# Kernel tuning notes

Measured on AMD Instinct MI355X. Metric: run time of the kernel, lower is better.

Reference implementation:

```python
import jax, jax.numpy as jnp
import numpy as np

N_HEAD = 16


def setup_inputs() -> dict:
    key = jax.random.key(0)
    ks = jax.random.split(key, 5)
    B, T, C = 4, 2048, 1024
    s = 0.02
    x = jax.random.normal(ks[0], (B, T, C), jnp.float32)
    wq = jax.random.normal(ks[1], (C, C), jnp.float32) * s
    wk = jax.random.normal(ks[2], (C, C), jnp.float32) * s
    wv = jax.random.normal(ks[3], (C, C), jnp.float32) * s
    wp = jax.random.normal(ks[4], (C, C), jnp.float32) * s
    zb = jnp.zeros((C,), jnp.float32)
    return {"x": x, "wq": wq, "bq": zb, "wk": wk, "bk": zb,
            "wv": wv, "bv": zb, "wp": wp, "bp": zb}


def _rope_cos_sin(T, D):
    half = D // 2
    i = jnp.arange(half, dtype=jnp.float32)
    alpha = 1.0 / (10000.0 ** (2.0 * i / D))        # [half]
    ang = jnp.arange(T, dtype=jnp.float32)[:, None] * alpha  # [T, half]
    return jnp.cos(ang), jnp.sin(ang)


def _apply_rope(t, cos, sin):
    # t: [B, H, T, D]; non-interleaved halves as in the torch module
    half = t.shape[-1] // 2
    xr, xi = t[..., :half], t[..., half:]
    return jnp.concatenate([xr * cos - xi * sin, xr * sin + xi * cos], axis=-1)


def reference(x, wq, bq, wk, bk, wv, bv, wp, bp):
    B, T, C = x.shape
    H = N_HEAD
    D = C // H
    # QKV projections (torch Linear: x @ W.T + b)
    def heads(w, b):
        return (x @ w.T + b).reshape(B, T, H, D).transpose(0, 2, 1, 3)
    q, k, v = heads(wq, bq), heads(wk, bk), heads(wv, bv)
    cos, sin = _rope_cos_sin(T, D)  # each [T, D//2], broadcasts over B,H
    q = _apply_rope(q, cos, sin)
    k = _apply_rope(k, cos, sin)
    scale = 1.0 / np.sqrt(D).astype(np.float32)
    att = jnp.einsum('bhtd,bhsd->bhts', q, k) * scale  # [B,H,T,T]
    causal = jnp.tril(jnp.ones((T, T), bool))
    att = jnp.where(causal, att, jnp.float32(-jnp.inf))
    att = jax.nn.softmax(att, axis=-1)
    y = jnp.einsum('bhts,bhsd->bhtd', att, v)  # [B,H,T,D]
    y = y.transpose(0, 2, 1, 3).reshape(B, T, C)
    return y @ wp.T + bp
```

## Files before the change

### kernel.cpp

```cpp
#include <hip/hip_runtime.h>
#include <math.h>

constexpr int B = 4, T = 2048, C = 1024, H = 16, D = 64;
constexpr int M = B * T;
constexpr size_t BTC = (size_t)B * T * C;
constexpr float QSCALE = 0.18033688011112042f;
constexpr float ROPE_C = -0.415241011861f;

typedef short bf16x8 __attribute__((ext_vector_type(8)));
typedef float f32x4 __attribute__((ext_vector_type(4)));

__device__ inline ushort f2bf(float f) {
  union { float f; unsigned u; } cv; cv.f = f;
  unsigned u = cv.u;
  u += 0x7fffu + ((u >> 16) & 1u);
  return (ushort)(u >> 16);
}
__device__ inline ushort f2bfr(float f) {
  union { float f; unsigned u; } cv; cv.f = f;
  return (ushort)((cv.u + 0x8000u) >> 16);
}

__device__ inline void async_load16(const void* g, void* l) {
  __builtin_amdgcn_global_load_lds(
      (const __attribute__((address_space(1))) void*)g,
      (__attribute__((address_space(3))) void*)l, 16, 0, 0);
}

__device__ __forceinline__ bf16x8 ones_frag() {
  bf16x8 v;
#pragma unroll
  for (int i = 0; i < 8; i++) v[i] = (short)0x3F80;
  return v;
}

__global__ __launch_bounds__(256) void conv_all(
    const float* __restrict__ x, const float* __restrict__ w0,
    const float* __restrict__ w1, const float* __restrict__ w2,
    const float* __restrict__ w3, ushort* __restrict__ xb,
    ushort* __restrict__ wb) {
  const int XBLK = (int)(BTC / 1024);
  const int WBLK = (C * C) / 1024;
  int blk = blockIdx.x;
  const float* src;
  ushort* dst;
  int i;
  if (blk < XBLK) {
    src = x; dst = xb;
    i = (blk * 256 + threadIdx.x) * 4;
  } else {
    int wseg = (blk - XBLK) >> 10;
    int wblk = (blk - XBLK) & (WBLK - 1);
    src = (wseg == 0) ? w0 : (wseg == 1) ? w1 : (wseg == 2) ? w2 : w3;
    dst = wb + (size_t)wseg * C * C;
    i = (wblk * 256 + threadIdx.x) * 4;
  }
  float4 v = *(const float4*)(src + i);
  ushort4 o;
  o.x = f2bf(v.x); o.y = f2bf(v.y); o.z = f2bf(v.z); o.w = f2bf(v.w);
  *(ushort4*)(dst + i) = o;
}

constexpr int QNT = C / 64;

template <int OM, int NCT>
__global__ __launch_bounds__(256, 2) void gemm_pipe(
    const ushort* __restrict__ A, const ushort* __restrict__ Wt,
    const float* __restrict__ b0, const float* __restrict__ b1,
    const float* __restrict__ b2, void* __restrict__ out1,
    void* __restrict__ out2, void* __restrict__ out3) {
  __shared__ ushort As[2][128 * 64] __attribute__((aligned(16)));
  __shared__ ushort Bs[3][128 * 64] __attribute__((aligned(16)));
  const int tid = threadIdx.x;
  const int lane = tid & 63;
  const int lrow = lane & 15, quad = lane >> 4;
  const int wave = tid >> 6;
  const int wr = wave >> 1, wc = wave & 1;
  const int x7 = lrow & 7;

  int bid = blockIdx.y * NCT + blockIdx.x;
  const int cpx = NCT * 8;
  int lin = (bid & 7) * cpx + (bid >> 3);
  int row0 = (lin / NCT) * 128;
  int col0 = (lin % NCT) * 128;

  unsigned gaA[4], gaB[4];
#pragma unroll
  for (int i = 0; i < 4; i++) {
    int c = tid + i * 256;
    int r = c >> 3, cl = c & 7;
    int g = (cl ^ (r & 7)) * 8;
    gaA[i] = (unsigned)(row0 + r) * C + g;
    gaB[i] = (unsigned)(col0 + r) * C + g;
  }

  f32x4 acc[4][4];
#pragma unroll
  for (int i = 0; i < 4; i++)
#pragma unroll
    for (int j = 0; j < 4; j++) acc[i][j] = (f32x4){0.f, 0.f, 0.f, 0.f};

#pragma unroll
  for (int i = 0; i < 4; i++)
    async_load16(A + gaA[i], &As[0][(tid + i * 256) * 8]);
#pragma unroll
  for (int i = 0; i < 4; i++)
    async_load16(Wt + gaB[i], &Bs[0][(tid + i * 256) * 8]);
#pragma unroll
  for (int i = 0; i < 4; i++)
    async_load16(Wt + gaB[i] + 64, &Bs[1][(tid + i * 256) * 8]);
  asm volatile("s_waitcnt vmcnt(4)" ::: "memory");
  __builtin_amdgcn_sched_barrier(0);
  __builtin_amdgcn_s_barrier();

  int bi = 0;
  for (int t = 0; t < QNT; ++t) {
    const int pa = t & 1;
    const ushort* Ap = As[pa];
    const ushort* Bp = Bs[bi];
    int bi2 = bi - 1; if (bi2 < 0) bi2 = 2;

    {
      const int slot = (quad ^ x7) * 8;
      bf16x8 aF[4], bF[4];
#pragma unroll
      for (int i = 0; i < 4; i++)
        aF[i] = *(const bf16x8*)&Ap[(wr * 64 + i * 16 + lrow) * 64 + slot];
#pragma unroll
      for (int j = 0; j < 4; j++)
        bF[j] = *(const bf16x8*)&Bp[(wc * 64 + j * 16 + lrow) * 64 + slot];
      if (t + 1 < QNT) {
#pragma unroll
        for (int i = 0; i < 4; i++)
          async_load16(A + gaA[i] + (t + 1) * 64,
                       &As[pa ^ 1][(tid + i * 256) * 8]);
      }
      __builtin_amdgcn_s_setprio(1);
#pragma unroll
      for (int i = 0; i < 4; i++)
#pragma unroll
        for (int j = 0; j < 4; j++)
          acc[i][j] = __builtin_amdgcn_mfma_f32_16x16x32_bf16(
              aF[i], bF[j], acc[i][j], 0, 0, 0);
      __builtin_amdgcn_s_setprio(0);
    }

    {
      const int slot = ((4 + quad) ^ x7) * 8;
      bf16x8 aF[4], bF[4];
#pragma unroll
      for (int i = 0; i < 4; i++)
        aF[i] = *(const bf16x8*)&Ap[(wr * 64 + i * 16 + lrow) * 64 + slot];
#pragma unroll
      for (int j = 0; j < 4; j++)
        bF[j] = *(const bf16x8*)&Bp[(wc * 64 + j * 16 + lrow) * 64 + slot];
      if (t + 2 < QNT) {
#pragma unroll
        for (int i = 0; i < 4; i++)
          async_load16(Wt + gaB[i] + (t + 2) * 64,
                       &Bs[bi2][(tid + i * 256) * 8]);
      }
      __builtin_amdgcn_s_setprio(1);
#pragma unroll
      for (int i = 0; i < 4; i++)
#pragma unroll
        for (int j = 0; j < 4; j++)
          acc[i][j] = __builtin_amdgcn_mfma_f32_16x16x32_bf16(
              aF[i], bF[j], acc[i][j], 0, 0, 0);
      __builtin_amdgcn_s_setprio(0);
    }

    if (t + 2 < QNT) {
      asm volatile("s_waitcnt vmcnt(4)" ::: "memory");
    } else {
      asm volatile("s_waitcnt vmcnt(0)" ::: "memory");
    }
    __builtin_amdgcn_sched_barrier(0);
    __builtin_amdgcn_s_barrier();
    bi = (bi == 2) ? 0 : bi + 1;
  }

  const int nb = col0 + wc * 64;
  const int mbase = row0 + wr * 64;
  const float* bias = (col0 < 1024) ? b0 : (col0 < 2048) ? b1 : b2;
  float bn[4];
#pragma unroll
  for (int j = 0; j < 4; j++) bn[j] = bias[(nb & 1023) + j * 16 + lrow];

  if (OM == 0) {
    const int N = C;
    float* outp = (float*)out1;
#pragma unroll
    for (int i = 0; i < 4; i++)
#pragma unroll
      for (int j = 0; j < 4; j++) {
        int n = nb + j * 16 + lrow;
#pragma unroll
        for (int r = 0; r < 4; r++) {
          int m = mbase + i * 16 + quad * 4 + r;
          outp[(size_t)m * N + n] = acc[i][j][r] + bn[j];
        }
      }
  } else {
    int seg = nb >> 10;
    int hh = (nb & 1023) >> 6;
    if (seg < 2) {
      ushort* dst = (seg == 0) ? (ushort*)out1 : (ushort*)out2;
      float scale = (seg == 0) ? QSCALE : 1.0f;
      float a0 = __builtin_amdgcn_exp2f((float)lrow * ROPE_C);
      float a1 = __builtin_amdgcn_exp2f((float)(lrow + 16) * ROPE_C);
#pragma unroll
      for (int i = 0; i < 4; i++) {
#pragma unroll
        for (int r = 0; r < 4; r++) {
          int m = mbase + i * 16 + quad * 4 + r;
          int tt = m & (T - 1), bb = m >> 11;
          float s0, c0, s1, c1;
          __sincosf((float)tt * a0, &s0, &c0);
          __sincosf((float)tt * a1, &s1, &c1);
          float xr0 = acc[i][0][r] + bn[0];
          float xi0 = acc[i][2][r] + bn[2];
          float xr1 = acc[i][1][r] + bn[1];
          float xi1 = acc[i][3][r] + bn[3];
          ushort* pp = dst + ((size_t)(bb * H + hh) * T + tt) * D + lrow;
          pp[0]  = f2bf((xr0 * c0 - xi0 * s0) * scale);
          pp[32] = f2bf((xr0 * s0 + xi0 * c0) * scale);
          pp[16] = f2bf((xr1 * c1 - xi1 * s1) * scale);
          pp[48] = f2bf((xr1 * s1 + xi1 * c1) * scale);
        }
      }
    } else {
      ushort* dst = (ushort*)out3;
#pragma unroll
      for (int i = 0; i < 4; i++) {
        int m0 = mbase + i * 16 + quad * 4;
        int t0 = m0 & (T - 1), bb = m0 >> 11;
        size_t base = (size_t)(bb * H + hh) * D * T + t0;
#pragma unroll
        for (int j = 0; j < 4; j++) {
          int d = j * 16 + lrow;
          ushort4 pk;
          pk.x = f2bf(acc[i][j][0] + bn[j]);
          pk.y = f2bf(acc[i][j][1] + bn[j]);
          pk.z = f2bf(acc[i][j][2] + bn[j]);
          pk.w = f2bf(acc[i][j][3] + bn[j]);
          *(ushort4*)(dst + base + (size_t)d * T) = pk;
        }
      }
    }
  }
}

__device__ __forceinline__ void stage_kv(
    const ushort* kbh, const ushort* vbh, int s0,
    ushort* Kl, ushort* Vl, int tid) {
#pragma unroll
  for (int i = 0; i < 2; i++) {
    int c = tid + i * 256;
    int r = c >> 3, cc = c & 7;
    int g = (cc ^ (r & 7)) * 8;
    async_load16(kbh + (size_t)(s0 + r) * D + g, Kl + c * 8);
    async_load16(vbh + (size_t)r * T + s0 + g, Vl + c * 8);
  }
}

template <int MODE>
__device__ __forceinline__ void attn_step4(
    int s0, const ushort* KL, const ushort* VL, ushort* P,
    const bf16x8 (&qf)[2][2], int lrow, int quad, int sw0, int sw1,
    int qg0, int qg1, f32x4 (&o)[4][2], f32x4 (&ol)[2]) {
  bf16x8 kf0[4], kf1[4];
#pragma unroll
  for (int kt = 0; kt < 4; kt++) {
    int base = (kt * 16 + lrow) * 64;
    kf0[kt] = *(const bf16x8*)&KL[base + sw0];
    kf1[kt] = *(const bf16x8*)&KL[base + sw1];
  }
  bf16x8 vf0[4], vf1[4];
#pragma unroll
  for (int ds = 0; ds < 4; ds++) {
    int base = (ds * 16 + lrow) * 64;
    vf0[ds] = *(const bf16x8*)&VL[base + sw0];
    vf1[ds] = *(const bf16x8*)&VL[base + sw1];
  }
#pragma unroll
  for (int g = 0; g < 2; g++) {
    if (MODE == 2 && g == 0) continue;
    int qg = g ? qg1 : qg0;
    f32x4 st[4];
    __builtin_amdgcn_s_setprio(1);
#pragma unroll
    for (int kt = 0; kt < 4; kt++) {
      f32x4 z = {0.f, 0.f, 0.f, 0.f};
      st[kt] = __builtin_amdgcn_mfma_f32_16x16x32_bf16(kf0[kt], qf[g][0], z, 0, 0, 0);
      st[kt] = __builtin_amdgcn_mfma_f32_16x16x32_bf16(kf1[kt], qf[g][1], st[kt], 0, 0, 0);
    }
    __builtin_amdgcn_s_setprio(0);
    if ((MODE == 1 && g == 0) || (MODE == 2 && g == 1)) {
#pragma unroll
      for (int kt = 0; kt < 4; kt++)
#pragma unroll
        for (int r = 0; r < 4; r++)
          if (s0 + kt * 16 + quad * 4 + r > qg) st[kt][r] = -1e30f;
    }
#pragma unroll
    for (int kt = 0; kt < 4; kt++) {
      ushort4 pk;
      pk.x = f2bfr(__builtin_amdgcn_exp2f(st[kt][0]));
      pk.y = f2bfr(__builtin_amdgcn_exp2f(st[kt][1]));
      pk.z = f2bfr(__builtin_amdgcn_exp2f(st[kt][2]));
      pk.w = f2bfr(__builtin_amdgcn_exp2f(st[kt][3]));
      *(ushort4*)&P[((2 * kt + (quad >> 1)) * 32 + g * 16 + lrow) * 8 + (quad & 1) * 4] = pk;
    }
  }
  asm volatile("" ::: "memory");
  bf16x8 ones = ones_frag();
#pragma unroll
  for (int g = 0; g < 2; g++) {
    if (MODE == 2 && g == 0) continue;
    bf16x8 pf0 = *(const bf16x8*)&P[(quad * 32 + g * 16 + lrow) * 8];
    bf16x8 pf1 = *(const bf16x8*)&P[((quad + 4) * 32 + g * 16 + lrow) * 8];
    __builtin_amdgcn_s_setprio(1);
    ol[g] = __builtin_amdgcn_mfma_f32_16x16x32_bf16(ones, pf0, ol[g], 0, 0, 0);
    ol[g] = __builtin_amdgcn_mfma_f32_16x16x32_bf16(ones, pf1, ol[g], 0, 0, 0);
#pragma unroll
    for (int ds = 0; ds < 4; ds++) {
      o[ds][g] = __builtin_amdgcn_mfma_f32_16x16x32_bf16(vf0[ds], pf0, o[ds][g], 0, 0, 0);
      o[ds][g] = __builtin_amdgcn_mfma_f32_16x16x32_bf16(vf1[ds], pf1, o[ds][g], 0, 0, 0);
    }
    __builtin_amdgcn_s_setprio(0);
  }
}

__global__ __launch_bounds__(256, 3) void attn_mfma4(
    const ushort* __restrict__ qb_, const ushort* __restrict__ kb_,
    const ushort* __restrict__ vtb_, ushort* __restrict__ y) {
  __shared__ ushort Kl[2][64 * 64] __attribute__((aligned(16)));
  __shared__ ushort Vl[2][64 * 64] __attribute__((aligned(16)));
  __shared__ ushort Pl[4][2048] __attribute__((aligned(16)));
  int tid = threadIdx.x;
  int wave = tid >> 6, lane = tid & 63;
  int lrow = lane & 15, quad = lane >> 4;
  int qbi = 15 - (int)(blockIdx.x >> 6);
  int bh = blockIdx.x & 63;
  int b = bh >> 4, h = bh & 15;
  int Q0 = qbi * 128;
  ushort* P = Pl[wave];
  const ushort* kbh = kb_ + (size_t)bh * T * D;
  const ushort* vbh = vtb_ + (size_t)bh * D * T;

  int qg0 = Q0 + wave * 16 + lrow;
  int qg1 = qg0 + 64;
  bf16x8 qf[2][2];
  {
    const ushort* qp0 = qb_ + ((size_t)bh * T + qg0) * D + quad * 8;
    qf[0][0] = *(const bf16x8*)qp0;
    qf[0][1] = *(const bf16x8*)(qp0 + 32);
    const ushort* qp1 = qb_ + ((size_t)bh * T + qg1) * D + quad * 8;
    qf[1][0] = *(const bf16x8*)qp1;
    qf[1][1] = *(const bf16x8*)(qp1 + 32);
  }
  int r7 = lrow & 7;
  int sw0 = (quad ^ r7) * 8;
  int sw1 = ((quad + 4) ^ r7) * 8;

  f32x4 o[4][2];
#pragma unroll
  for (int ds = 0; ds < 4; ds++)
#pragma unroll
    for (int g = 0; g < 2; g++) o[ds][g] = (f32x4){0.f, 0.f, 0.f, 0.f};
  f32x4 ol[2] = {(f32x4){0.f, 0.f, 0.f, 0.f}, (f32x4){0.f, 0.f, 0.f, 0.f}};

  int trips = 2 * qbi + 2;
  stage_kv(kbh, vbh, 0, Kl[0], Vl[0], tid);
  int it = 0;
  for (; it < trips - 2; ++it) {
    __syncthreads();
    stage_kv(kbh, vbh, (it + 1) * 64, Kl[(it + 1) & 1], Vl[(it + 1) & 1], tid);
    attn_step4<0>(it * 64, Kl[it & 1], Vl[it & 1], P, qf, lrow, quad, sw0, sw1,
                  qg0, qg1, o, ol);
  }
  __syncthreads();
  stage_kv(kbh, vbh, (it + 1) * 64, Kl[(it + 1) & 1], Vl[(it + 1) & 1], tid);
  attn_step4<1>(it * 64, Kl[it & 1], Vl[it & 1], P, qf, lrow, quad, sw0, sw1,
                qg0, qg1, o, ol);
  ++it;
  __syncthreads();
  attn_step4<2>(it * 64, Kl[it & 1], Vl[it & 1], P, qf, lrow, quad, sw0, sw1,
                qg0, qg1, o, ol);

#pragma unroll
  for (int g = 0; g < 2; g++) {
    float inv = 1.f / ol[g][0];
    int qg = g ? qg1 : qg0;
#pragma unroll
    for (int ds = 0; ds < 4; ds++) {
      ushort4 pk;
      pk.x = f2bf(o[ds][g][0] * inv);
      pk.y = f2bf(o[ds][g][1] * inv);
      pk.z = f2bf(o[ds][g][2] * inv);
      pk.w = f2bf(o[ds][g][3] * inv);
      *(ushort4*)(y + ((size_t)b * T + qg) * C + h * D + ds * 16 + quad * 4) = pk;
    }
  }
}

extern "C" void kernel_launch(void* const* d_in, const int* in_sizes, int n_in,
                              void* d_out, int out_size, void* d_ws, size_t ws_size,
                              hipStream_t stream) {
  const float* x  = (const float*)d_in[0];
  const float* wq = (const float*)d_in[1];
  const float* bq = (const float*)d_in[2];
  const float* wk = (const float*)d_in[3];
  const float* bk = (const float*)d_in[4];
  const float* wv = (const float*)d_in[5];
  const float* bv = (const float*)d_in[6];
  const float* wp = (const float*)d_in[7];
  const float* bp = (const float*)d_in[8];
  float* out = (float*)d_out;

  ushort* xb    = (ushort*)d_ws;
  ushort* qb    = xb + BTC;
  ushort* kb    = qb + BTC;
  ushort* vtb   = kb + BTC;
  ushort* yb    = vtb + BTC;
  ushort* wqkvb = yb + BTC;
  ushort* wpb   = wqkvb + (size_t)3 * C * C;

  conv_all<<<(int)(BTC / 1024) + 4 * (C * C) / 1024, 256, 0, stream>>>(
      x, wq, wk, wv, wp, xb, wqkvb);

  dim3 qkv_grid(3 * C / 128, M / 128);
  gemm_pipe<1, 24><<<qkv_grid, 256, 0, stream>>>(
      xb, wqkvb, bq, bk, bv, qb, kb, vtb);

  attn_mfma4<<<(B * H * T / 128), 256, 0, stream>>>(qb, kb, vtb, yb);

  dim3 proj_grid(C / 128, M / 128);
  gemm_pipe<0, 8><<<proj_grid, 256, 0, stream>>>(
      yb, wpb, bp, bp, bp, out, nullptr, nullptr);
}
```

Measured before the change: 231.3 us.

## Split QKV GEMM into transposed-operand Q/K kernel and separate V kernel

The fused QKV projection is split into two launches. A new Q/K GEMM swaps the MFMA operand roles so each lane holds consecutive head-dim values, which lets the RoPE epilogue write packed 4-element bf16 stores instead of scattered 2-byte stores. V is handled by the existing template in its own launch. This removes the uncoalesced epilogue writes for Q and K, at the cost of an extra kernel launch and a smaller per-launch grid for V that may fill the GPU less well.

```diff
diff --git a/kernel.cpp b/kernel.cpp
--- a/kernel.cpp
+++ b/kernel.cpp
@@ -63,12 +63,168 @@
 
 constexpr int QNT = C / 64;
 
+__global__ __launch_bounds__(256, 2) void gemm_qk(
+    const ushort* __restrict__ A, const ushort* __restrict__ Wt,
+    const float* __restrict__ bq, const float* __restrict__ bk,
+    ushort* __restrict__ outq, ushort* __restrict__ outk) {
+  __shared__ ushort As[2][128 * 64] __attribute__((aligned(16)));
+  __shared__ ushort Bs[3][128 * 64] __attribute__((aligned(16)));
+  const int tid = threadIdx.x;
+  const int lane = tid & 63;
+  const int lrow = lane & 15, quad = lane >> 4;
+  const int wave = tid >> 6;
+  const int wm = wave >> 1, wn = wave & 1;
+  const int x7 = lrow & 7;
+
+  int bid = blockIdx.y * 16 + blockIdx.x;
+  int lin = (bid & 7) * 128 + (bid >> 3);
+  int row0 = (lin >> 4) * 128;
+  int col0 = (lin & 15) * 128;
+
+  unsigned gaA[4], gaB[4];
+#pragma unroll
+  for (int i = 0; i < 4; i++) {
+    int c = tid + i * 256;
+    int r = c >> 3, cl = c & 7;
+    int g = (cl ^ (r & 7)) * 8;
+    gaA[i] = (unsigned)(row0 + r) * C + g;
+    gaB[i] = (unsigned)(col0 + r) * C + g;
+  }
+
+  f32x4 acc[4][4];
+#pragma unroll
+  for (int i = 0; i < 4; i++)
+#pragma unroll
+    for (int j = 0; j < 4; j++) acc[i][j] = (f32x4){0.f, 0.f, 0.f, 0.f};
+
+#pragma unroll
+  for (int i = 0; i < 4; i++)
+    async_load16(A + gaA[i], &As[0][(tid + i * 256) * 8]);
+#pragma unroll
+  for (int i = 0; i < 4; i++)
+    async_load16(Wt + gaB[i], &Bs[0][(tid + i * 256) * 8]);
+#pragma unroll
+  for (int i = 0; i < 4; i++)
+    async_load16(Wt + gaB[i] + 64, &Bs[1][(tid + i * 256) * 8]);
+  asm volatile("s_waitcnt vmcnt(4)" ::: "memory");
+  __builtin_amdgcn_sched_barrier(0);
+  __builtin_amdgcn_s_barrier();
+
+  int bi = 0;
+  for (int t = 0; t < QNT; ++t) {
+    const int pa = t & 1;
+    const ushort* Ap = As[pa];
+    const ushort* Bp = Bs[bi];
+    int bi2 = bi - 1; if (bi2 < 0) bi2 = 2;
+
+    {
+      const int slot = (quad ^ x7) * 8;
+      bf16x8 aF[4], bF[4];
+#pragma unroll
+      for (int i = 0; i < 4; i++)
+        aF[i] = *(const bf16x8*)&Bp[(wn * 64 + i * 16 + lrow) * 64 + slot];
+#pragma unroll
+      for (int j = 0; j < 4; j++)
+        bF[j] = *(const bf16x8*)&Ap[(wm * 64 + j * 16 + lrow) * 64 + slot];
+      if (t + 1 < QNT) {
+#pragma unroll
+        for (int i = 0; i < 4; i++)
+          async_load16(A + gaA[i] + (t + 1) * 64,
+                       &As[pa ^ 1][(tid + i * 256) * 8]);
+      }
+      __builtin_amdgcn_s_setprio(1);
+#pragma unroll
+      for (int i = 0; i < 4; i++)
+#pragma unroll
+        for (int j = 0; j < 4; j++)
+          acc[i][j] = __builtin_amdgcn_mfma_f32_16x16x32_bf16(
+              aF[i], bF[j], acc[i][j], 0, 0, 0);
+      __builtin_amdgcn_s_setprio(0);
+    }
+
+    {
+      const int slot = ((4 + quad) ^ x7) * 8;
+      bf16x8 aF[4], bF[4];
+#pragma unroll
+      for (int i = 0; i < 4; i++)
+        aF[i] = *(const bf16x8*)&Bp[(wn * 64 + i * 16 + lrow) * 64 + slot];
+#pragma unroll
+      for (int j = 0; j < 4; j++)
+        bF[j] = *(const bf16x8*)&Ap[(wm * 64 + j * 16 + lrow) * 64 + slot];
+      if (t + 2 < QNT) {
+#pragma unroll
+        for (int i = 0; i < 4; i++)
+          async_load16(Wt + gaB[i] + (t + 2) * 64,
+                       &Bs[bi2][(tid + i * 256) * 8]);
+      }
+      __builtin_amdgcn_s_setprio(1);
+#pragma unroll
+      for (int i = 0; i < 4; i++)
+#pragma unroll
+        for (int j = 0; j < 4; j++)
+          acc[i][j] = __builtin_amdgcn_mfma_f32_16x16x32_bf16(
+              aF[i], bF[j], acc[i][j], 0, 0, 0);
+      __builtin_amdgcn_s_setprio(0);
+    }
+
+    if (t + 2 < QNT) {
+      asm volatile("s_waitcnt vmcnt(4)" ::: "memory");
+    } else {
+      asm volatile("s_waitcnt vmcnt(0)" ::: "memory");
+    }
+    __builtin_amdgcn_sched_barrier(0);
+    __builtin_amdgcn_s_barrier();
+    bi = (bi == 2) ? 0 : bi + 1;
+  }
+
+  const int nbase = col0 + wn * 64;
+  ushort* dst = (nbase < 1024) ? outq : outk;
+  const float* bias = (nbase < 1024) ? bq : bk;
+  const float scale = (nbase < 1024) ? QSCALE : 1.0f;
+  const int hh = (nbase & 1023) >> 6;
+  const int bb = row0 >> 11;
+  const int tb = (row0 & (T - 1)) + wm * 64;
+
+  f32x4 bn[4];
+#pragma unroll
+  for (int i = 0; i < 4; i++)
+    bn[i] = *(const f32x4*)&bias[(nbase & 1023) + i * 16 + quad * 4];
+  float af[2][4];
+#pragma unroll
+  for (int i2 = 0; i2 < 2; i2++)
+#pragma unroll
+    for (int r = 0; r < 4; r++)
+      af[i2][r] = __builtin_amdgcn_exp2f((float)(i2 * 16 + quad * 4 + r) * ROPE_C);
+
+#pragma unroll
+  for (int j = 0; j < 4; j++) {
+    int tt = tb + j * 16 + lrow;
+    size_t rb = ((size_t)(bb * H + hh) * T + tt) * D;
+#pragma unroll
+    for (int i2 = 0; i2 < 2; i2++) {
+      ushort4 ul, uh;
+      float lo[4], hi[4];
+#pragma unroll
+      for (int r = 0; r < 4; r++) {
+        float s, c;
+        __sincosf((float)tt * af[i2][r], &s, &c);
+        float xr = acc[i2][j][r] + bn[i2][r];
+        float xi = acc[i2 + 2][j][r] + bn[i2 + 2][r];
+        lo[r] = (xr * c - xi * s) * scale;
+        hi[r] = (xr * s + xi * c) * scale;
+      }
+      ul.x = f2bf(lo[0]); ul.y = f2bf(lo[1]); ul.z = f2bf(lo[2]); ul.w = f2bf(lo[3]);
+      uh.x = f2bf(hi[0]); uh.y = f2bf(hi[1]); uh.z = f2bf(hi[2]); uh.w = f2bf(hi[3]);
+      *(ushort4*)(dst + rb + i2 * 16 + quad * 4) = ul;
+      *(ushort4*)(dst + rb + (i2 + 2) * 16 + quad * 4) = uh;
+    }
+  }
+}
+
 template <int OM, int NCT>
 __global__ __launch_bounds__(256, 2) void gemm_pipe(
     const ushort* __restrict__ A, const ushort* __restrict__ Wt,
-    const float* __restrict__ b0, const float* __restrict__ b1,
-    const float* __restrict__ b2, void* __restrict__ out1,
-    void* __restrict__ out2, void* __restrict__ out3) {
+    const float* __restrict__ bias_, void* __restrict__ out1) {
   __shared__ ushort As[2][128 * 64] __attribute__((aligned(16)));
   __shared__ ushort Bs[3][128 * 64] __attribute__((aligned(16)));
   const int tid = threadIdx.x;
@@ -182,10 +338,9 @@
 
   const int nb = col0 + wc * 64;
   const int mbase = row0 + wr * 64;
-  const float* bias = (col0 < 1024) ? b0 : (col0 < 2048) ? b1 : b2;
   float bn[4];
 #pragma unroll
-  for (int j = 0; j < 4; j++) bn[j] = bias[(nb & 1023) + j * 16 + lrow];
+  for (int j = 0; j < 4; j++) bn[j] = bias_[(nb & 1023) + j * 16 + lrow];
 
   if (OM == 0) {
     const int N = C;
@@ -202,50 +357,22 @@
         }
       }
   } else {
-    int seg = nb >> 10;
     int hh = (nb & 1023) >> 6;
-    if (seg < 2) {
-      ushort* dst = (seg == 0) ? (ushort*)out1 : (ushort*)out2;
-      float scale = (seg == 0) ? QSCALE : 1.0f;
-      float a0 = __builtin_amdgcn_exp2f((float)lrow * ROPE_C);
-      float a1 = __builtin_amdgcn_exp2f((float)(lrow + 16) * ROPE_C);
-#pragma unroll
-      for (int i = 0; i < 4; i++) {
-#pragma unroll
-        for (int r = 0; r < 4; r++) {
-          int m = mbase + i * 16 + quad * 4 + r;
-          int tt = m & (T - 1), bb = m >> 11;
-          float s0, c0, s1, c1;
-          __sincosf((float)tt * a0, &s0, &c0);
-          __sincosf((float)tt * a1, &s1, &c1);
-          float xr0 = acc[i][0][r] + bn[0];
-          float xi0 = acc[i][2][r] + bn[2];
-          float xr1 = acc[i][1][r] + bn[1];
-          float xi1 = acc[i][3][r] + bn[3];
-          ushort* pp = dst + ((size_t)(bb * H + hh) * T + tt) * D + lrow;
-          pp[0]  = f2bf((xr0 * c0 - xi0 * s0) * scale);
-          pp[32] = f2bf((xr0 * s0 + xi0 * c0) * scale);
-          pp[16] = f2bf((xr1 * c1 - xi1 * s1) * scale);
-          pp[48] = f2bf((xr1 * s1 + xi1 * c1) * scale);
-        }
-      }
-    } else {
-      ushort* dst = (ushort*)out3;
-#pragma unroll
-      for (int i = 0; i < 4; i++) {
-        int m0 = mbase + i * 16 + quad * 4;
-        int t0 = m0 & (T - 1), bb = m0 >> 11;
-        size_t base = (size_t)(bb * H + hh) * D * T + t0;
-#pragma unroll
-        for (int j = 0; j < 4; j++) {
-          int d = j * 16 + lrow;
-          ushort4 pk;
-          pk.x = f2bf(acc[i][j][0] + bn[j]);
-          pk.y = f2bf(acc[i][j][1] + bn[j]);
-          pk.z = f2bf(acc[i][j][2] + bn[j]);
-          pk.w = f2bf(acc[i][j][3] + bn[j]);
-          *(ushort4*)(dst + base + (size_t)d * T) = pk;
-        }
+    ushort* dst = (ushort*)out1;
+#pragma unroll
+    for (int i = 0; i < 4; i++) {
+      int m0 = mbase + i * 16 + quad * 4;
+      int t0 = m0 & (T - 1), bb = m0 >> 11;
+      size_t base = (size_t)(bb * H + hh) * D * T + t0;
+#pragma unroll
+      for (int j = 0; j < 4; j++) {
+        int d = j * 16 + lrow;
+        ushort4 pk;
+        pk.x = f2bf(acc[i][j][0] + bn[j]);
+        pk.y = f2bf(acc[i][j][1] + bn[j]);
+        pk.z = f2bf(acc[i][j][2] + bn[j]);
+        pk.w = f2bf(acc[i][j][3] + bn[j]);
+        *(ushort4*)(dst + base + (size_t)d * T) = pk;
       }
     }
   }
@@ -430,13 +557,14 @@
   conv_all<<<(int)(BTC / 1024) + 4 * (C * C) / 1024, 256, 0, stream>>>(
       x, wq, wk, wv, wp, xb, wqkvb);
 
-  dim3 qkv_grid(3 * C / 128, M / 128);
-  gemm_pipe<1, 24><<<qkv_grid, 256, 0, stream>>>(
-      xb, wqkvb, bq, bk, bv, qb, kb, vtb);
+  dim3 qk_grid(16, M / 128);
+  gemm_qk<<<qk_grid, 256, 0, stream>>>(xb, wqkvb, bq, bk, qb, kb);
+
+  dim3 v_grid(8, M / 128);
+  gemm_pipe<2, 8><<<v_grid, 256, 0, stream>>>(
+      xb, wqkvb + (size_t)2048 * C, bv, vtb);
 
   attn_mfma4<<<(B * H * T / 128), 256, 0, stream>>>(qb, kb, vtb, yb);
 
-  dim3 proj_grid(C / 128, M / 128);
-  gemm_pipe<0, 8><<<proj_grid, 256, 0, stream>>>(
-      yb, wpb, bp, bp, bp, out, nullptr, nullptr);
-}
+  gemm_pipe<0, 8><<<v_grid, 256, 0, stream>>>(yb, wpb, bp, out);
+}
```

Result: slower. 237.3 us (+2.6%).
